# Performance work log

Measured on AMD Instinct MI355X. Metric: run time of the kernel, lower is better.

## Reference

```python
import jax, jax.numpy as jnp
import numpy as np

B, N, C = 128, 100, 32
HE = 32          # n_hidden_edge
FILTERS = [64, 64, 64]
OUT = 16


def setup_inputs() -> dict:
    key = jax.random.key(0)
    ks = jax.random.split(key, 16)
    x = jax.random.normal(ks[0], (B, N, C), dtype=jnp.float32)
    A = jax.random.uniform(ks[1], (B, N, N), dtype=jnp.float32)
    A = 0.5 * (A + A.transpose(0, 2, 1))  # symmetric adjacency
    mask = jnp.ones((B, N), dtype=jnp.float32)

    def lin(k, fin, fout):
        return jax.random.normal(k, (fin, fout), dtype=jnp.float32) / np.sqrt(fin).astype(np.float32)

    # edge_pred: Linear(2C -> HE), ReLU, Linear(HE -> 1)
    ew1 = lin(ks[2], 2 * C, HE); eb1 = jnp.zeros((HE,), jnp.float32)
    ew2 = lin(ks[3], HE, 1)[:, 0]; eb2 = jnp.zeros((), jnp.float32)
    # gconv layers: in = prev*2 relations (input A + predicted A)
    gw0 = lin(ks[4], C * 2, FILTERS[0]); gb0 = jnp.zeros((FILTERS[0],), jnp.float32)
    gw1 = lin(ks[5], FILTERS[0] * 2, FILTERS[1]); gb1 = jnp.zeros((FILTERS[1],), jnp.float32)
    gw2 = lin(ks[6], FILTERS[1] * 2, FILTERS[2]); gb2 = jnp.zeros((FILTERS[2],), jnp.float32)
    # final classifier (dropout is identity in eval mode)
    fw = lin(ks[7], FILTERS[2], OUT); fb = jnp.zeros((OUT,), jnp.float32)
    return dict(x=x, A=A, mask=mask, ew1=ew1, eb1=eb1, ew2=ew2, eb2=eb2,
                gw0=gw0, gb0=gb0, gw1=gw1, gb1=gb1, gw2=gw2, gb2=gb2, fw=fw, fb=fb)


def _laplacian(Ar):
    # K=1: A_hat = A + I; L = D^-1/2 A_hat D^-1/2 with D from sum over dim 1
    n = Ar.shape[1]
    A_hat = Ar + jnp.eye(n, dtype=Ar.dtype)[None]
    D = (jnp.sum(A_hat, axis=1) + 1e-5) ** (-0.5)  # [B,N]
    return D[:, :, None] * A_hat * D[:, None, :]


def reference(x, A, mask, ew1, eb1, ew2, eb2, gw0, gb0, gw1, gb1, gw2, gb2, fw, fb):
    Bv, Nv, Cv = x.shape
    # --- edge prediction over all valid pairs i<j (vectorized gather-MLP-scatter) ---
    # concat(x_i, x_j) @ ew1 factored: x_i @ ew1[:C] + x_j @ ew1[C:]
    hi = x @ ew1[:Cv]            # [B,N,HE]
    hj = x @ ew1[Cv:]            # [B,N,HE]
    pre = hi[:, :, None, :] + hj[:, None, :, :] + eb1      # [B,N,N,HE]
    h = jax.nn.relu(pre) @ ew2 + eb2                        # [B,N,N], h[b,i,j]=MLP([x_i,x_j])
    y = jnp.exp(0.5 * (h + h.transpose(0, 2, 1)))           # symmetric score
    valid = mask[:, :, None] * mask[:, None, :]
    triu = jnp.triu(jnp.ones((Nv, Nv), dtype=x.dtype), k=1)
    A_u = y * valid * triu                                  # scatter into upper triangle
    A_pred = A_u + A_u.transpose(0, 2, 1)

    # two relations: original A and predicted A
    L0 = _laplacian(A)
    L1 = _laplacian(A_pred)

    h = x
    for (W, b) in ((gw0, gb0), (gw1, gb1), (gw2, gb2)):
        xh = jnp.concatenate([L0 @ h, L1 @ h], axis=2)      # [B,N,2*F_in]
        h = jax.nn.relu((xh @ W + b) * mask[:, :, None])
    pooled = jnp.max(h, axis=1)                             # [B,F]
    return pooled @ fw + fb                                 # [B,OUT]
```

## Files before the change

### kernel.cpp

```cpp
#include <hip/hip_runtime.h>

#define NN 100
#define CC 32
#define HEE 32
#define FF 64
#define TILE 10

typedef float f32x4 __attribute__((ext_vector_type(4)));
typedef __bf16 bf16x8 __attribute__((ext_vector_type(8)));
#define MFMA16 __builtin_amdgcn_mfma_f32_16x16x32_bf16

union FragU {
  unsigned short s[8];
  bf16x8 v;
  float4 f4;
};

static __device__ __forceinline__ void split2(float v, unsigned short& h, unsigned short& l) {
  union { float f; unsigned u; } c; c.f = v;
  unsigned r = c.u + 0x7FFF + ((c.u >> 16) & 1);
  unsigned short hs = (unsigned short)(r >> 16);
  union { unsigned u; float f; } hb; hb.u = ((unsigned)hs) << 16;
  float rem = v - hb.f;
  union { float f; unsigned u; } c2; c2.f = rem;
  unsigned r2 = c2.u + 0x7FFF + ((c2.u >> 16) & 1);
  h = hs; l = (unsigned short)(r2 >> 16);
}

__global__ __launch_bounds__(64) void k_hidden(
    const float* __restrict__ x, const float* __restrict__ A,
    const float* __restrict__ ew1, const float* __restrict__ eb1,
    float* __restrict__ hi, float* __restrict__ hj, float* __restrict__ d0) {
  int bn = blockIdx.x;
  int t = threadIdx.x;
  __shared__ float xr[CC];
  if (t < CC) xr[t] = x[bn * CC + t];

  const float* arow = A + (size_t)bn * NN;
  float s = 0.f;
  for (int j = t; j < NN; j += 64) s += arow[j];
#pragma unroll
  for (int off = 32; off > 0; off >>= 1) s += __shfl_down(s, off);
  if (t == 0) d0[bn] = 1.0f / sqrtf(s + 1.0f + 1e-5f);

  __syncthreads();
  int k = t & 31;
  const float* w = ew1 + (t < 32 ? 0 : CC * HEE) + k;
  float acc = (t < 32) ? eb1[k] : 0.f;
#pragma unroll
  for (int c = 0; c < CC; ++c) acc += xr[c] * w[c * HEE];
  if (t < 32) hi[bn * HEE + k] = acc;
  else        hj[bn * HEE + k] = acc;
}

__global__ __launch_bounds__(256) void k_edge(
    const float* __restrict__ hi, const float* __restrict__ hj,
    const float* __restrict__ ew2, const float* __restrict__ eb2,
    const float* __restrict__ mask,
    float* __restrict__ Ahat1, float* __restrict__ d1) {
  __shared__ __align__(16) float shi[NN * HEE];
  __shared__ __align__(16) float shj[NN * HEE];
  __shared__ __align__(16) float sw2[HEE];
  __shared__ float sm[NN];
  __shared__ float sA[TILE][NN];
  int t = threadIdx.x;
  int b = blockIdx.x / 10;
  int i0 = (blockIdx.x % 10) * TILE;

  const float4* hi4 = (const float4*)(hi + (size_t)b * NN * HEE);
  const float4* hj4 = (const float4*)(hj + (size_t)b * NN * HEE);
  float4* shi4 = (float4*)shi;
  float4* shj4 = (float4*)shj;
  for (int v = t; v < NN * 8; v += 256) {
    int j = v >> 3, k4 = v & 7;
    int sw = (j << 3) | (k4 ^ (j & 7));
    shi4[sw] = hi4[v];
    shj4[sw] = hj4[v];
  }
  if (t < HEE) sw2[t] = ew2[t];
  if (t < NN) sm[t] = mask[b * NN + t];
  __syncthreads();

  float e2 = eb2[0];
  float4* sw24 = (float4*)sw2;
  for (int p = t; p < TILE * NN; p += 256) {
    int r = p / NN, j = p % NN, i = i0 + r;
    float val;
    if (j == i) {
      val = 1.0f;
    } else {
      float a1 = 0.f, a2 = 0.f;
#pragma unroll
      for (int k4 = 0; k4 < 8; ++k4) {
        float4 hii = shi4[(i << 3) | (k4 ^ (i & 7))];
        float4 hji = shj4[(i << 3) | (k4 ^ (i & 7))];
        float4 hij = shi4[(j << 3) | (k4 ^ (j & 7))];
        float4 hjj = shj4[(j << 3) | (k4 ^ (j & 7))];
        float4 w4 = sw24[k4];
        a1 += fmaxf(hii.x + hjj.x, 0.f) * w4.x;
        a2 += fmaxf(hij.x + hji.x, 0.f) * w4.x;
        a1 += fmaxf(hii.y + hjj.y, 0.f) * w4.y;
        a2 += fmaxf(hij.y + hji.y, 0.f) * w4.y;
        a1 += fmaxf(hii.z + hjj.z, 0.f) * w4.z;
        a2 += fmaxf(hij.z + hji.z, 0.f) * w4.z;
        a1 += fmaxf(hii.w + hjj.w, 0.f) * w4.w;
        a2 += fmaxf(hij.w + hji.w, 0.f) * w4.w;
      }
      val = expf(0.5f * (a1 + a2) + e2) * sm[i] * sm[j];
    }
    sA[r][j] = val;
    Ahat1[((size_t)b * NN + i) * NN + j] = val;
  }
  __syncthreads();
  if (t < TILE) {
    float s = 0.f;
    for (int j = 0; j < NN; ++j) s += sA[t][j];
    d1[b * NN + i0 + t] = 1.0f / sqrtf(s + 1e-5f);
  }
}

__global__ __launch_bounds__(256) void k_fmtL(
    const float* __restrict__ A, const float* __restrict__ Ahat1,
    const float* __restrict__ d0, const float* __restrict__ d1,
    float* __restrict__ Limg) {
  int gid = blockIdx.x * 256 + threadIdx.x;
  int lane = gid & 63;
  int frag = gid >> 6;
  int b = frag / 56;
  int r = frag % 56;
  int mt = r >> 3, kt = r & 7;
  int m = mt * 16 + (lane & 15);
  int o = lane >> 4;
  int rel = kt >> 2;
  int jb = (kt & 3) * 32 + o * 8;

  float v[8];
  if (m < NN) {
    if (rel == 0) {
      float di = d0[b * NN + m];
      const float* Ar = A + ((size_t)b * NN + m) * NN;
#pragma unroll
      for (int e = 0; e < 8; ++e) {
        int j = jb + e;
        v[e] = (j < NN) ? di * (Ar[j] + (j == m ? 1.f : 0.f)) * d0[b * NN + j] : 0.f;
      }
    } else {
      float di = d1[b * NN + m];
      const float* Ar = Ahat1 + ((size_t)b * NN + m) * NN;
#pragma unroll
      for (int e = 0; e < 8; ++e) {
        int j = jb + e;
        v[e] = (j < NN) ? di * Ar[j] * d1[b * NN + j] : 0.f;
      }
    }
  } else {
#pragma unroll
    for (int e = 0; e < 8; ++e) v[e] = 0.f;
  }
  FragU hh, ll;
#pragma unroll
  for (int e = 0; e < 8; ++e) split2(v[e], hh.s[e], ll.s[e]);
  char* dst = (char*)Limg + (size_t)frag * 2048 + lane * 16;
  *(float4*)dst = hh.f4;
  *(float4*)(dst + 1024) = ll.f4;
}

__global__ __launch_bounds__(256) void k_fmtW(
    const float* __restrict__ gw1, const float* __restrict__ gw2,
    float* __restrict__ Wimg) {
  int gid = blockIdx.x * 256 + threadIdx.x;
  int lane = gid & 63;
  int frag = gid >> 6;
  int wsel = frag >> 4;
  int rr = frag & 15;
  int kt2 = rr >> 3, nt2 = rr & 7;
  int n = nt2 * 16 + (lane & 15);
  int rel = n >> 6, f = n & 63;
  int kb = kt2 * 32 + (lane >> 4) * 8;
  const float* W = wsel ? gw2 : gw1;
  FragU hh, ll;
#pragma unroll
  for (int e = 0; e < 8; ++e) {
    float v = W[(size_t)(rel * 64 + kb + e) * 64 + f];
    split2(v, hh.s[e], ll.s[e]);
  }
  char* dst = (char*)Wimg + (size_t)frag * 2048 + lane * 16;
  *(float4*)dst = hh.f4;
  *(float4*)(dst + 1024) = ll.f4;
}

__global__ __launch_bounds__(256, 2) void k_preP(
    const float* __restrict__ x, const float* __restrict__ gw0,
    float* __restrict__ Pimg) {
  int t = threadIdx.x;
  int b = blockIdx.x & 127;
  int q = blockIdx.x >> 7;
  int wid = __builtin_amdgcn_readfirstlane(t >> 6);
  int lane = t & 63;
  int rg = wid * 4 + q;
  int row0 = rg * 8;
  if (row0 >= NN) return;

  int rowc[8];
#pragma unroll
  for (int r = 0; r < 8; ++r) rowc[r] = min(row0 + r, NN - 1);

  float acc0[8], acc1[8];
#pragma unroll
  for (int r = 0; r < 8; ++r) { acc0[r] = 0.f; acc1[r] = 0.f; }

  for (int c4 = 0; c4 < CC / 4; ++c4) {
    int c = c4 * 4;
    float w00 = gw0[(size_t)c * 64 + lane];
    float w01 = gw0[(size_t)(c + 1) * 64 + lane];
    float w02 = gw0[(size_t)(c + 2) * 64 + lane];
    float w03 = gw0[(size_t)(c + 3) * 64 + lane];
    float w10 = gw0[(size_t)(CC + c) * 64 + lane];
    float w11 = gw0[(size_t)(CC + c + 1) * 64 + lane];
    float w12 = gw0[(size_t)(CC + c + 2) * 64 + lane];
    float w13 = gw0[(size_t)(CC + c + 3) * 64 + lane];
#pragma unroll
    for (int r = 0; r < 8; ++r) {
      float4 a4 = *(const float4*)(x + ((size_t)b * NN + rowc[r]) * CC + c);
      acc0[r] += a4.x * w00 + a4.y * w01 + a4.z * w02 + a4.w * w03;
      acc1[r] += a4.x * w10 + a4.y * w11 + a4.z * w12 + a4.w * w13;
    }
  }
#pragma unroll
  for (int r = 0; r < 8; ++r) {
    if (row0 + r >= NN) { acc0[r] = 0.f; acc1[r] = 0.f; }
  }
  int o_t = (row0 & 31) >> 3;
  int lane_t = o_t * 16 + (lane & 15);
  int nt_t = lane >> 4;
  FragU h0, l0, h1, l1;
#pragma unroll
  for (int r = 0; r < 8; ++r) {
    split2(acc0[r], h0.s[r], l0.s[r]);
    split2(acc1[r], h1.s[r], l1.s[r]);
  }
  char* base = (char*)Pimg + (size_t)b * 65536;
  int kt0 = row0 >> 5;
  char* dp0 = base + (size_t)(kt0 * 4 + nt_t) * 2048 + lane_t * 16;
  *(float4*)dp0 = h0.f4;
  *(float4*)(dp0 + 1024) = l0.f4;
  char* dp1 = base + (size_t)((4 + kt0) * 4 + nt_t) * 2048 + lane_t * 16;
  *(float4*)dp1 = h1.f4;
  *(float4*)(dp1 + 1024) = l1.f4;
}

template <int LAST>
__global__ __launch_bounds__(256, 2) void k_gmm1(
    const float* __restrict__ Limg, const float* __restrict__ Pimg,
    const float* __restrict__ bias, const float* __restrict__ mask,
    float* __restrict__ outbuf, float* __restrict__ pooled) {
  __shared__ float pm[4][16];
  int t = threadIdx.x;
  int b = blockIdx.x >> 2;
  int q = blockIdx.x & 3;
  int h = q >> 1, np = q & 1;
  int w = __builtin_amdgcn_readfirstlane(t >> 6);
  int lane = t & 63;
  int nt = np * 2 + (w & 1);
  int mt0 = h * 3 + (w >> 1) * 2;
  int mt1 = mt0 + 1;

  const char* Lb = (const char*)Limg + (size_t)b * 114688;
  const char* Pb = (const char*)Pimg + (size_t)b * 65536;

  f32x4 acc0 = {0.f, 0.f, 0.f, 0.f};
  f32x4 acc1 = {0.f, 0.f, 0.f, 0.f};
#pragma unroll
  for (int kt = 0; kt < 8; ++kt) {
    FragU bh, bl, a0h, a0l, a1h, a1l;
    const char* pp = Pb + (size_t)(kt * 4 + nt) * 2048 + lane * 16;
    bh.f4 = *(const float4*)pp;
    bl.f4 = *(const float4*)(pp + 1024);
    const char* l0p = Lb + (size_t)(mt0 * 8 + kt) * 2048 + lane * 16;
    const char* l1p = Lb + (size_t)(mt1 * 8 + kt) * 2048 + lane * 16;
    a0h.f4 = *(const float4*)l0p;
    a0l.f4 = *(const float4*)(l0p + 1024);
    a1h.f4 = *(const float4*)l1p;
    a1l.f4 = *(const float4*)(l1p + 1024);
    acc0 = MFMA16(a0h.v, bh.v, acc0, 0, 0, 0);
    acc1 = MFMA16(a1h.v, bh.v, acc1, 0, 0, 0);
    acc0 = MFMA16(a0l.v, bh.v, acc0, 0, 0, 0);
    acc1 = MFMA16(a1l.v, bh.v, acc1, 0, 0, 0);
    acc0 = MFMA16(a0h.v, bl.v, acc0, 0, 0, 0);
    acc1 = MFMA16(a1h.v, bl.v, acc1, 0, 0, 0);
  }

  int f = nt * 16 + (lane & 15);
  float biasf = bias[f];
  const float* mb = mask + b * NN;
  int rbase = (lane >> 4) * 4;
  float mx = 0.f;

#pragma unroll
  for (int reg = 0; reg < 4; ++reg) {
    int gi = mt0 * 16 + rbase + reg;
    float v = 0.f;
    if (gi < NN) v = fmaxf((acc0[reg] + biasf) * mb[gi], 0.f);
    if (!LAST) outbuf[((size_t)b * 112 + gi) * 64 + f] = v;
    else mx = fmaxf(mx, v);
  }
#pragma unroll
  for (int reg = 0; reg < 4; ++reg) {
    int gi = mt1 * 16 + rbase + reg;
    float v = 0.f;
    if (gi < NN) v = fmaxf((acc1[reg] + biasf) * mb[gi], 0.f);
    if (!LAST) outbuf[((size_t)b * 112 + gi) * 64 + f] = v;
    else mx = fmaxf(mx, v);
  }

  if (LAST) {
    mx = fmaxf(mx, __shfl_xor(mx, 16));
    mx = fmaxf(mx, __shfl_xor(mx, 32));
    if (lane < 16) pm[w][lane] = mx;
    __syncthreads();
    if (w < 2 && lane < 16) {
      float m2 = fmaxf(pm[w][lane], pm[w + 2][lane]);
      pooled[((size_t)b * 2 + h) * 64 + (np * 2 + w) * 16 + lane] = m2;
    }
  }
}

__global__ __launch_bounds__(256, 2) void k_gmm2(
    const float* __restrict__ outbuf, const float* __restrict__ Wimg,
    float* __restrict__ Pimg_out) {
  int t = threadIdx.x;
  int b = blockIdx.x >> 2;
  int q2 = blockIdx.x & 3;
  int h = q2 >> 1, nh = q2 & 1;
  int w = __builtin_amdgcn_readfirstlane(t >> 6);
  int lane = t & 63;
  int nt2 = nh * 4 + w;
  int o = lane >> 4;
  int ml = lane & 15;

  f32x4 acc[4];
#pragma unroll
  for (int l = 0; l < 4; ++l) acc[l] = (f32x4){0.f, 0.f, 0.f, 0.f};

#pragma unroll
  for (int kt2 = 0; kt2 < 2; ++kt2) {
    FragU bh, bl;
    const char* wp = (const char*)Wimg + (size_t)(kt2 * 8 + nt2) * 2048 + lane * 16;
    bh.f4 = *(const float4*)wp;
    bl.f4 = *(const float4*)(wp + 1024);
    int kb = kt2 * 32 + o * 8;
#pragma unroll
    for (int l = 0; l < 4; ++l) {
      int m = (h * 3 + l) * 16 + ml;
      const float* op = outbuf + ((size_t)b * 112 + m) * 64 + kb;
      float4 v0 = *(const float4*)op;
      float4 v1 = *(const float4*)(op + 4);
      float vv[8] = {v0.x, v0.y, v0.z, v0.w, v1.x, v1.y, v1.z, v1.w};
      FragU ah, al;
#pragma unroll
      for (int e = 0; e < 8; ++e) split2(vv[e], ah.s[e], al.s[e]);
      acc[l] = MFMA16(ah.v, bh.v, acc[l], 0, 0, 0);
      acc[l] = MFMA16(al.v, bh.v, acc[l], 0, 0, 0);
      acc[l] = MFMA16(ah.v, bl.v, acc[l], 0, 0, 0);
    }
  }

  int nprime = nt2 * 16 + ml;
  int rel = nprime >> 6;
  int f = nprime & 63;
  int nt_t = f >> 4;
  char* Pout = (char*)Pimg_out + (size_t)b * 65536;
#pragma unroll
  for (int l = 0; l < 4; ++l) {
    int i0 = (h * 3 + l) * 16 + (lane >> 4) * 4;
    int kt_ = (rel * 128 + i0) >> 5;
    int o_t = ((rel * 128 + i0) & 31) >> 3;
    int e0 = i0 & 7;
    unsigned short hs[4], ls[4];
#pragma unroll
    for (int reg = 0; reg < 4; ++reg) split2(acc[l][reg], hs[reg], ls[reg]);
    ushort4 hv = {hs[0], hs[1], hs[2], hs[3]};
    ushort4 lv = {ls[0], ls[1], ls[2], ls[3]};
    char* dst = Pout + (size_t)(kt_ * 4 + nt_t) * 2048 + (o_t * 16 + (f & 15)) * 16 + e0 * 2;
    *(ushort4*)dst = hv;
    *(ushort4*)(dst + 1024) = lv;
  }
}

__global__ __launch_bounds__(64) void k_final(
    const float* __restrict__ pooled, const float* __restrict__ fw,
    const float* __restrict__ fb, float* __restrict__ out) {
  int b = blockIdx.x;
  int t = threadIdx.x;
  __shared__ float sp[FF];
  float m = fmaxf(pooled[(size_t)b * 128 + t], pooled[(size_t)b * 128 + 64 + t]);
  sp[t] = m;
  __syncthreads();
  if (t < 16) {
    float acc = fb[t];
#pragma unroll
    for (int f = 0; f < FF; ++f) acc += sp[f] * fw[f * 16 + t];
    out[b * 16 + t] = acc;
  }
}

extern "C" void kernel_launch(void* const* d_in, const int* in_sizes, int n_in,
                              void* d_out, int out_size, void* d_ws, size_t ws_size,
                              hipStream_t stream) {
  const float* x    = (const float*)d_in[0];
  const float* A    = (const float*)d_in[1];
  const float* mask = (const float*)d_in[2];
  const float* ew1  = (const float*)d_in[3];
  const float* eb1  = (const float*)d_in[4];
  const float* ew2  = (const float*)d_in[5];
  const float* eb2  = (const float*)d_in[6];
  const float* gw0  = (const float*)d_in[7];
  const float* gb0  = (const float*)d_in[8];
  const float* gw1  = (const float*)d_in[9];
  const float* gb1  = (const float*)d_in[10];
  const float* gw2  = (const float*)d_in[11];
  const float* gb2  = (const float*)d_in[12];
  const float* fw   = (const float*)d_in[13];
  const float* fb   = (const float*)d_in[14];
  float* out = (float*)d_out;
  float* ws = (float*)d_ws;

  const int B = 128;
  float* hi   = ws;
  float* hj   = hi + 409600;
  float* Ah1  = hj + 409600;
  float* d0   = Ah1 + 1280000;
  float* d1   = d0 + 12800;
  float* Limg = d1 + 12800;
  float* PA   = Limg + 3670016;
  float* PB   = PA + 2097152;
  float* Wimg = PB + 2097152;
  float* outb = Wimg + 16384;
  float* pooled = outb + 917504;

  k_hidden<<<B * NN, 64, 0, stream>>>(x, A, ew1, eb1, hi, hj, d0);
  k_edge<<<B * 10, 256, 0, stream>>>(hi, hj, ew2, eb2, mask, Ah1, d1);
  k_fmtW<<<8, 256, 0, stream>>>(gw1, gw2, Wimg);
  k_preP<<<512, 256, 0, stream>>>(x, gw0, PA);
  k_fmtL<<<1792, 256, 0, stream>>>(A, Ah1, d0, d1, Limg);

  k_gmm1<0><<<512, 256, 0, stream>>>(Limg, PA, gb0, mask, outb, pooled);
  k_gmm2<<<512, 256, 0, stream>>>(outb, (const float*)Wimg, PB);
  k_gmm1<0><<<512, 256, 0, stream>>>(Limg, PB, gb1, mask, outb, pooled);
  k_gmm2<<<512, 256, 0, stream>>>(outb, (const float*)((const char*)Wimg + 32768), PA);
  k_gmm1<1><<<512, 256, 0, stream>>>(Limg, PA, gb2, mask, outb, pooled);

  k_final<<<B, 64, 0, stream>>>(pooled, fw, fb, out);
}
```

Before: 92.61 us.

## Fuse prep kernels and merge per-layer graph GEMM with weight GEMM

Merges k_hidden, k_fmtW and k_preP into one k_combo launch, with k_hidden now handling four nodes per 256-thread block. k_edge is restructured so each 32-lane group owns one row, keeps the i-row hidden vectors in registers, and computes degree sums with shuffles instead of a serial loop. The two GEMM kernels per layer are fused into k_layer: the L·P result for a 16-row tile is staged in swizzled LDS and multiplied by the next weight image in place, removing the outbuf round trip and two launches. Pooling now writes seven partial maxima per batch, which k_final reduces. The trade-off is less MFMA work per block (one accumulator per wave) and some duplicated LDS staging.

Measured after the change: 101.3 us. 1.09x slower.

```diff
diff --git a/kernel.cpp b/kernel.cpp
--- a/kernel.cpp
+++ b/kernel.cpp
@@ -27,33 +27,122 @@
   h = hs; l = (unsigned short)(r2 >> 16);
 }
 
-__global__ __launch_bounds__(64) void k_hidden(
+__global__ __launch_bounds__(256) void k_combo(
     const float* __restrict__ x, const float* __restrict__ A,
     const float* __restrict__ ew1, const float* __restrict__ eb1,
-    float* __restrict__ hi, float* __restrict__ hj, float* __restrict__ d0) {
-  int bn = blockIdx.x;
+    const float* __restrict__ gw0, const float* __restrict__ gw1,
+    const float* __restrict__ gw2,
+    float* __restrict__ hi, float* __restrict__ hj, float* __restrict__ d0,
+    float* __restrict__ Wimg, float* __restrict__ Pimg) {
+  int blk = blockIdx.x;
   int t = threadIdx.x;
-  __shared__ float xr[CC];
-  if (t < CC) xr[t] = x[bn * CC + t];
-
-  const float* arow = A + (size_t)bn * NN;
-  float s = 0.f;
-  for (int j = t; j < NN; j += 64) s += arow[j];
-#pragma unroll
-  for (int off = 32; off > 0; off >>= 1) s += __shfl_down(s, off);
-  if (t == 0) d0[bn] = 1.0f / sqrtf(s + 1.0f + 1e-5f);
-
-  __syncthreads();
-  int k = t & 31;
-  const float* w = ew1 + (t < 32 ? 0 : CC * HEE) + k;
-  float acc = (t < 32) ? eb1[k] : 0.f;
-#pragma unroll
-  for (int c = 0; c < CC; ++c) acc += xr[c] * w[c * HEE];
-  if (t < 32) hi[bn * HEE + k] = acc;
-  else        hj[bn * HEE + k] = acc;
-}
-
-__global__ __launch_bounds__(256) void k_edge(
+
+  if (blk < 3200) {
+    __shared__ float xr[4][CC];
+    int wid = t >> 6, lane = t & 63;
+    int bn = blk * 4 + wid;
+    if (lane < CC) xr[wid][lane] = x[bn * CC + lane];
+
+    const float* arow = A + (size_t)bn * NN;
+    float s = arow[lane] + (lane < NN - 64 ? arow[lane + 64] : 0.f);
+#pragma unroll
+    for (int off = 32; off > 0; off >>= 1) s += __shfl_down(s, off);
+    if (lane == 0) d0[bn] = 1.0f / sqrtf(s + 1.0f + 1e-5f);
+    __syncthreads();
+
+    int k = lane & 31;
+    const float* w = ew1 + (lane < 32 ? 0 : CC * HEE) + k;
+    float acc = (lane < 32) ? eb1[k] : 0.f;
+#pragma unroll
+    for (int c = 0; c < CC; ++c) acc += xr[wid][c] * w[c * HEE];
+    if (lane < 32) hi[bn * HEE + k] = acc;
+    else           hj[bn * HEE + k] = acc;
+    return;
+  }
+
+  if (blk < 3208) {
+    int gid = (blk - 3200) * 256 + t;
+    int lane = gid & 63;
+    int frag = gid >> 6;
+    int wsel = frag >> 4;
+    int rr = frag & 15;
+    int kt2 = rr >> 3, nt2 = rr & 7;
+    int n = nt2 * 16 + (lane & 15);
+    int rel = n >> 6, f = n & 63;
+    int kb = kt2 * 32 + (lane >> 4) * 8;
+    const float* W = wsel ? gw2 : gw1;
+    FragU hh, ll;
+#pragma unroll
+    for (int e = 0; e < 8; ++e) {
+      float v = W[(size_t)(rel * 64 + kb + e) * 64 + f];
+      split2(v, hh.s[e], ll.s[e]);
+    }
+    char* dst = (char*)Wimg + (size_t)frag * 2048 + lane * 16;
+    *(float4*)dst = hh.f4;
+    *(float4*)(dst + 1024) = ll.f4;
+    return;
+  }
+
+  {
+    int idx = blk - 3208;
+    int b = idx & 127;
+    int q = idx >> 7;
+    int wid = t >> 6;
+    int lane = t & 63;
+    int rg = wid * 4 + q;
+    int row0 = rg * 8;
+    if (row0 >= NN) return;
+
+    int rowc[8];
+#pragma unroll
+    for (int r = 0; r < 8; ++r) rowc[r] = min(row0 + r, NN - 1);
+
+    float acc0[8], acc1[8];
+#pragma unroll
+    for (int r = 0; r < 8; ++r) { acc0[r] = 0.f; acc1[r] = 0.f; }
+
+    for (int c4 = 0; c4 < CC / 4; ++c4) {
+      int c = c4 * 4;
+      float w00 = gw0[(size_t)c * 64 + lane];
+      float w01 = gw0[(size_t)(c + 1) * 64 + lane];
+      float w02 = gw0[(size_t)(c + 2) * 64 + lane];
+      float w03 = gw0[(size_t)(c + 3) * 64 + lane];
+      float w10 = gw0[(size_t)(CC + c) * 64 + lane];
+      float w11 = gw0[(size_t)(CC + c + 1) * 64 + lane];
+      float w12 = gw0[(size_t)(CC + c + 2) * 64 + lane];
+      float w13 = gw0[(size_t)(CC + c + 3) * 64 + lane];
+#pragma unroll
+      for (int r = 0; r < 8; ++r) {
+        float4 a4 = *(const float4*)(x + ((size_t)b * NN + rowc[r]) * CC + c);
+        acc0[r] += a4.x * w00 + a4.y * w01 + a4.z * w02 + a4.w * w03;
+        acc1[r] += a4.x * w10 + a4.y * w11 + a4.z * w12 + a4.w * w13;
+      }
+    }
+#pragma unroll
+    for (int r = 0; r < 8; ++r) {
+      if (row0 + r >= NN) { acc0[r] = 0.f; acc1[r] = 0.f; }
+    }
+    int o_t = (row0 & 31) >> 3;
+    int lane_t = o_t * 16 + (lane & 15);
+    int nt_t = lane >> 4;
+    FragU h0, l0, h1, l1;
+#pragma unroll
+    for (int r = 0; r < 8; ++r) {
+      split2(acc0[r], h0.s[r], l0.s[r]);
+      split2(acc1[r], h1.s[r], l1.s[r]);
+    }
+    char* base = (char*)Pimg + (size_t)b * 65536;
+    int kt0 = row0 >> 5;
+    char* dp0 = base + (size_t)(kt0 * 4 + nt_t) * 2048 + lane_t * 16;
+    *(float4*)dp0 = h0.f4;
+    *(float4*)(dp0 + 1024) = l0.f4;
+    char* dp1 = base + (size_t)((4 + kt0) * 4 + nt_t) * 2048 + lane_t * 16;
+    *(float4*)dp1 = h1.f4;
+    *(float4*)(dp1 + 1024) = l1.f4;
+  }
+}
+
+__global__ __launch_bounds__(320) void k_edge(
     const float* __restrict__ hi, const float* __restrict__ hj,
     const float* __restrict__ ew2, const float* __restrict__ eb2,
     const float* __restrict__ mask,
@@ -62,7 +151,7 @@
   __shared__ __align__(16) float shj[NN * HEE];
   __shared__ __align__(16) float sw2[HEE];
   __shared__ float sm[NN];
-  __shared__ float sA[TILE][NN];
+  __shared__ float sA[TILE][NN + 4];
   int t = threadIdx.x;
   int b = blockIdx.x / 10;
   int i0 = (blockIdx.x % 10) * TILE;
@@ -71,7 +160,7 @@
   const float4* hj4 = (const float4*)(hj + (size_t)b * NN * HEE);
   float4* shi4 = (float4*)shi;
   float4* shj4 = (float4*)shj;
-  for (int v = t; v < NN * 8; v += 256) {
+  for (int v = t; v < NN * 8; v += 320) {
     int j = v >> 3, k4 = v & 7;
     int sw = (j << 3) | (k4 ^ (j & 7));
     shi4[sw] = hi4[v];
@@ -81,42 +170,55 @@
   if (t < NN) sm[t] = mask[b * NN + t];
   __syncthreads();
 
+  int r = t >> 5, jl = t & 31;
+  int i = i0 + r;
+  float4* sw24 = (float4*)sw2;
+
+  float4 hii[8], hji[8];
+#pragma unroll
+  for (int k4 = 0; k4 < 8; ++k4) {
+    int sw = (i << 3) | (k4 ^ (i & 7));
+    hii[k4] = shi4[sw];
+    hji[k4] = shj4[sw];
+  }
   float e2 = eb2[0];
-  float4* sw24 = (float4*)sw2;
-  for (int p = t; p < TILE * NN; p += 256) {
-    int r = p / NN, j = p % NN, i = i0 + r;
-    float val;
-    if (j == i) {
-      val = 1.0f;
-    } else {
+  float mi = sm[i];
+  float* Ar = Ahat1 + ((size_t)b * NN + i) * NN;
+
+#pragma unroll
+  for (int s = 0; s < 4; ++s) {
+    int j = jl + 32 * s;
+    if (j < NN) {
       float a1 = 0.f, a2 = 0.f;
 #pragma unroll
       for (int k4 = 0; k4 < 8; ++k4) {
-        float4 hii = shi4[(i << 3) | (k4 ^ (i & 7))];
-        float4 hji = shj4[(i << 3) | (k4 ^ (i & 7))];
-        float4 hij = shi4[(j << 3) | (k4 ^ (j & 7))];
-        float4 hjj = shj4[(j << 3) | (k4 ^ (j & 7))];
+        int sw = (j << 3) | (k4 ^ (j & 7));
+        float4 hjjK = shj4[sw];
+        float4 hijK = shi4[sw];
         float4 w4 = sw24[k4];
-        a1 += fmaxf(hii.x + hjj.x, 0.f) * w4.x;
-        a2 += fmaxf(hij.x + hji.x, 0.f) * w4.x;
-        a1 += fmaxf(hii.y + hjj.y, 0.f) * w4.y;
-        a2 += fmaxf(hij.y + hji.y, 0.f) * w4.y;
-        a1 += fmaxf(hii.z + hjj.z, 0.f) * w4.z;
-        a2 += fmaxf(hij.z + hji.z, 0.f) * w4.z;
-        a1 += fmaxf(hii.w + hjj.w, 0.f) * w4.w;
-        a2 += fmaxf(hij.w + hji.w, 0.f) * w4.w;
+        float4 hiiK = hii[k4], hjiK = hji[k4];
+        a1 += fmaxf(hiiK.x + hjjK.x, 0.f) * w4.x;
+        a2 += fmaxf(hijK.x + hjiK.x, 0.f) * w4.x;
+        a1 += fmaxf(hiiK.y + hjjK.y, 0.f) * w4.y;
+        a2 += fmaxf(hijK.y + hjiK.y, 0.f) * w4.y;
+        a1 += fmaxf(hiiK.z + hjjK.z, 0.f) * w4.z;
+        a2 += fmaxf(hijK.z + hjiK.z, 0.f) * w4.z;
+        a1 += fmaxf(hiiK.w + hjjK.w, 0.f) * w4.w;
+        a2 += fmaxf(hijK.w + hjiK.w, 0.f) * w4.w;
       }
-      val = expf(0.5f * (a1 + a2) + e2) * sm[i] * sm[j];
-    }
-    sA[r][j] = val;
-    Ahat1[((size_t)b * NN + i) * NN + j] = val;
+      float val = (j == i) ? 1.0f
+                           : expf(0.5f * (a1 + a2) + e2) * mi * sm[j];
+      sA[r][j] = val;
+      Ar[j] = val;
+    }
   }
   __syncthreads();
-  if (t < TILE) {
-    float s = 0.f;
-    for (int j = 0; j < NN; ++j) s += sA[t][j];
-    d1[b * NN + i0 + t] = 1.0f / sqrtf(s + 1e-5f);
-  }
+
+  float s2 = sA[r][jl] + sA[r][jl + 32] + sA[r][jl + 64] +
+             (jl < NN - 96 ? sA[r][jl + 96] : 0.f);
+#pragma unroll
+  for (int off = 16; off > 0; off >>= 1) s2 += __shfl_down(s2, off, 32);
+  if (jl == 0) d1[b * NN + i] = 1.0f / sqrtf(s2 + 1e-5f);
 }
 
 __global__ __launch_bounds__(256) void k_fmtL(
@@ -165,223 +267,112 @@
   *(float4*)(dst + 1024) = ll.f4;
 }
 
-__global__ __launch_bounds__(256) void k_fmtW(
-    const float* __restrict__ gw1, const float* __restrict__ gw2,
-    float* __restrict__ Wimg) {
-  int gid = blockIdx.x * 256 + threadIdx.x;
-  int lane = gid & 63;
-  int frag = gid >> 6;
-  int wsel = frag >> 4;
-  int rr = frag & 15;
-  int kt2 = rr >> 3, nt2 = rr & 7;
-  int n = nt2 * 16 + (lane & 15);
-  int rel = n >> 6, f = n & 63;
-  int kb = kt2 * 32 + (lane >> 4) * 8;
-  const float* W = wsel ? gw2 : gw1;
-  FragU hh, ll;
-#pragma unroll
-  for (int e = 0; e < 8; ++e) {
-    float v = W[(size_t)(rel * 64 + kb + e) * 64 + f];
-    split2(v, hh.s[e], ll.s[e]);
-  }
-  char* dst = (char*)Wimg + (size_t)frag * 2048 + lane * 16;
-  *(float4*)dst = hh.f4;
-  *(float4*)(dst + 1024) = ll.f4;
-}
-
-__global__ __launch_bounds__(256, 2) void k_preP(
-    const float* __restrict__ x, const float* __restrict__ gw0,
-    float* __restrict__ Pimg) {
-  int t = threadIdx.x;
-  int b = blockIdx.x & 127;
-  int q = blockIdx.x >> 7;
-  int wid = __builtin_amdgcn_readfirstlane(t >> 6);
-  int lane = t & 63;
-  int rg = wid * 4 + q;
-  int row0 = rg * 8;
-  if (row0 >= NN) return;
-
-  int rowc[8];
-#pragma unroll
-  for (int r = 0; r < 8; ++r) rowc[r] = min(row0 + r, NN - 1);
-
-  float acc0[8], acc1[8];
-#pragma unroll
-  for (int r = 0; r < 8; ++r) { acc0[r] = 0.f; acc1[r] = 0.f; }
-
-  for (int c4 = 0; c4 < CC / 4; ++c4) {
-    int c = c4 * 4;
-    float w00 = gw0[(size_t)c * 64 + lane];
-    float w01 = gw0[(size_t)(c + 1) * 64 + lane];
-    float w02 = gw0[(size_t)(c + 2) * 64 + lane];
-    float w03 = gw0[(size_t)(c + 3) * 64 + lane];
-    float w10 = gw0[(size_t)(CC + c) * 64 + lane];
-    float w11 = gw0[(size_t)(CC + c + 1) * 64 + lane];
-    float w12 = gw0[(size_t)(CC + c + 2) * 64 + lane];
-    float w13 = gw0[(size_t)(CC + c + 3) * 64 + lane];
-#pragma unroll
-    for (int r = 0; r < 8; ++r) {
-      float4 a4 = *(const float4*)(x + ((size_t)b * NN + rowc[r]) * CC + c);
-      acc0[r] += a4.x * w00 + a4.y * w01 + a4.z * w02 + a4.w * w03;
-      acc1[r] += a4.x * w10 + a4.y * w11 + a4.z * w12 + a4.w * w13;
-    }
-  }
-#pragma unroll
-  for (int r = 0; r < 8; ++r) {
-    if (row0 + r >= NN) { acc0[r] = 0.f; acc1[r] = 0.f; }
-  }
-  int o_t = (row0 & 31) >> 3;
-  int lane_t = o_t * 16 + (lane & 15);
-  int nt_t = lane >> 4;
-  FragU h0, l0, h1, l1;
-#pragma unroll
-  for (int r = 0; r < 8; ++r) {
-    split2(acc0[r], h0.s[r], l0.s[r]);
-    split2(acc1[r], h1.s[r], l1.s[r]);
-  }
-  char* base = (char*)Pimg + (size_t)b * 65536;
-  int kt0 = row0 >> 5;
-  char* dp0 = base + (size_t)(kt0 * 4 + nt_t) * 2048 + lane_t * 16;
-  *(float4*)dp0 = h0.f4;
-  *(float4*)(dp0 + 1024) = l0.f4;
-  char* dp1 = base + (size_t)((4 + kt0) * 4 + nt_t) * 2048 + lane_t * 16;
-  *(float4*)dp1 = h1.f4;
-  *(float4*)(dp1 + 1024) = l1.f4;
-}
-
 template <int LAST>
-__global__ __launch_bounds__(256, 2) void k_gmm1(
+__global__ __launch_bounds__(256) void k_layer(
     const float* __restrict__ Limg, const float* __restrict__ Pimg,
     const float* __restrict__ bias, const float* __restrict__ mask,
-    float* __restrict__ outbuf, float* __restrict__ pooled) {
-  __shared__ float pm[4][16];
+    const char* __restrict__ Wimg, float* __restrict__ Pout,
+    float* __restrict__ pooled) {
+  __shared__ __align__(16) float sO[16 * 64];
   int t = threadIdx.x;
-  int b = blockIdx.x >> 2;
-  int q = blockIdx.x & 3;
-  int h = q >> 1, np = q & 1;
-  int w = __builtin_amdgcn_readfirstlane(t >> 6);
+  int b = blockIdx.x / 7;
+  int mt = blockIdx.x % 7;
+  int w = t >> 6;
   int lane = t & 63;
-  int nt = np * 2 + (w & 1);
-  int mt0 = h * 3 + (w >> 1) * 2;
-  int mt1 = mt0 + 1;
+  int nt = w;
 
   const char* Lb = (const char*)Limg + (size_t)b * 114688;
   const char* Pb = (const char*)Pimg + (size_t)b * 65536;
 
-  f32x4 acc0 = {0.f, 0.f, 0.f, 0.f};
-  f32x4 acc1 = {0.f, 0.f, 0.f, 0.f};
+  f32x4 acc = {0.f, 0.f, 0.f, 0.f};
 #pragma unroll
   for (int kt = 0; kt < 8; ++kt) {
-    FragU bh, bl, a0h, a0l, a1h, a1l;
+    FragU bh, bl, ah, al;
     const char* pp = Pb + (size_t)(kt * 4 + nt) * 2048 + lane * 16;
     bh.f4 = *(const float4*)pp;
     bl.f4 = *(const float4*)(pp + 1024);
-    const char* l0p = Lb + (size_t)(mt0 * 8 + kt) * 2048 + lane * 16;
-    const char* l1p = Lb + (size_t)(mt1 * 8 + kt) * 2048 + lane * 16;
-    a0h.f4 = *(const float4*)l0p;
-    a0l.f4 = *(const float4*)(l0p + 1024);
-    a1h.f4 = *(const float4*)l1p;
-    a1l.f4 = *(const float4*)(l1p + 1024);
-    acc0 = MFMA16(a0h.v, bh.v, acc0, 0, 0, 0);
-    acc1 = MFMA16(a1h.v, bh.v, acc1, 0, 0, 0);
-    acc0 = MFMA16(a0l.v, bh.v, acc0, 0, 0, 0);
-    acc1 = MFMA16(a1l.v, bh.v, acc1, 0, 0, 0);
-    acc0 = MFMA16(a0h.v, bl.v, acc0, 0, 0, 0);
-    acc1 = MFMA16(a1h.v, bl.v, acc1, 0, 0, 0);
+    const char* lp = Lb + (size_t)(mt * 8 + kt) * 2048 + lane * 16;
+    ah.f4 = *(const float4*)lp;
+    al.f4 = *(const float4*)(lp + 1024);
+    acc = MFMA16(ah.v, bh.v, acc, 0, 0, 0);
+    acc = MFMA16(al.v, bh.v, acc, 0, 0, 0);
+    acc = MFMA16(ah.v, bl.v, acc, 0, 0, 0);
   }
 
   int f = nt * 16 + (lane & 15);
   float biasf = bias[f];
   const float* mb = mask + b * NN;
   int rbase = (lane >> 4) * 4;
-  float mx = 0.f;
-
+  float vv[4];
 #pragma unroll
   for (int reg = 0; reg < 4; ++reg) {
-    int gi = mt0 * 16 + rbase + reg;
-    float v = 0.f;
-    if (gi < NN) v = fmaxf((acc0[reg] + biasf) * mb[gi], 0.f);
-    if (!LAST) outbuf[((size_t)b * 112 + gi) * 64 + f] = v;
-    else mx = fmaxf(mx, v);
-  }
-#pragma unroll
-  for (int reg = 0; reg < 4; ++reg) {
-    int gi = mt1 * 16 + rbase + reg;
-    float v = 0.f;
-    if (gi < NN) v = fmaxf((acc1[reg] + biasf) * mb[gi], 0.f);
-    if (!LAST) outbuf[((size_t)b * 112 + gi) * 64 + f] = v;
-    else mx = fmaxf(mx, v);
+    int gi = mt * 16 + rbase + reg;
+    vv[reg] = (gi < NN) ? fmaxf((acc[reg] + biasf) * mb[gi], 0.f) : 0.f;
   }
 
   if (LAST) {
+    float mx = fmaxf(fmaxf(vv[0], vv[1]), fmaxf(vv[2], vv[3]));
     mx = fmaxf(mx, __shfl_xor(mx, 16));
     mx = fmaxf(mx, __shfl_xor(mx, 32));
-    if (lane < 16) pm[w][lane] = mx;
-    __syncthreads();
-    if (w < 2 && lane < 16) {
-      float m2 = fmaxf(pm[w][lane], pm[w + 2][lane]);
-      pooled[((size_t)b * 2 + h) * 64 + (np * 2 + w) * 16 + lane] = m2;
-    }
-  }
-}
-
-__global__ __launch_bounds__(256, 2) void k_gmm2(
-    const float* __restrict__ outbuf, const float* __restrict__ Wimg,
-    float* __restrict__ Pimg_out) {
-  int t = threadIdx.x;
-  int b = blockIdx.x >> 2;
-  int q2 = blockIdx.x & 3;
-  int h = q2 >> 1, nh = q2 & 1;
-  int w = __builtin_amdgcn_readfirstlane(t >> 6);
-  int lane = t & 63;
-  int nt2 = nh * 4 + w;
-  int o = lane >> 4;
-  int ml = lane & 15;
-
-  f32x4 acc[4];
-#pragma unroll
-  for (int l = 0; l < 4; ++l) acc[l] = (f32x4){0.f, 0.f, 0.f, 0.f};
-
+    if (lane < 16) pooled[((size_t)b * 7 + mt) * 64 + w * 16 + lane] = mx;
+    return;
+  }
+
+#pragma unroll
+  for (int reg = 0; reg < 4; ++reg) {
+    int lr2 = rbase + reg;
+    sO[lr2 * 64 + ((((f >> 3) ^ (lr2 & 7)) << 3) | (f & 7))] = vv[reg];
+  }
+  __syncthreads();
+
+  int ml = lane & 15, o = lane >> 4;
+  f32x4 accE0 = {0.f, 0.f, 0.f, 0.f};
+  f32x4 accE1 = {0.f, 0.f, 0.f, 0.f};
 #pragma unroll
   for (int kt2 = 0; kt2 < 2; ++kt2) {
-    FragU bh, bl;
-    const char* wp = (const char*)Wimg + (size_t)(kt2 * 8 + nt2) * 2048 + lane * 16;
-    bh.f4 = *(const float4*)wp;
-    bl.f4 = *(const float4*)(wp + 1024);
-    int kb = kt2 * 32 + o * 8;
-#pragma unroll
-    for (int l = 0; l < 4; ++l) {
-      int m = (h * 3 + l) * 16 + ml;
-      const float* op = outbuf + ((size_t)b * 112 + m) * 64 + kb;
-      float4 v0 = *(const float4*)op;
-      float4 v1 = *(const float4*)(op + 4);
-      float vv[8] = {v0.x, v0.y, v0.z, v0.w, v1.x, v1.y, v1.z, v1.w};
-      FragU ah, al;
-#pragma unroll
-      for (int e = 0; e < 8; ++e) split2(vv[e], ah.s[e], al.s[e]);
-      acc[l] = MFMA16(ah.v, bh.v, acc[l], 0, 0, 0);
-      acc[l] = MFMA16(al.v, bh.v, acc[l], 0, 0, 0);
-      acc[l] = MFMA16(ah.v, bl.v, acc[l], 0, 0, 0);
-    }
-  }
-
-  int nprime = nt2 * 16 + ml;
-  int rel = nprime >> 6;
-  int f = nprime & 63;
-  int nt_t = f >> 4;
-  char* Pout = (char*)Pimg_out + (size_t)b * 65536;
-#pragma unroll
-  for (int l = 0; l < 4; ++l) {
-    int i0 = (h * 3 + l) * 16 + (lane >> 4) * 4;
-    int kt_ = (rel * 128 + i0) >> 5;
-    int o_t = ((rel * 128 + i0) & 31) >> 3;
-    int e0 = i0 & 7;
+    int c = kt2 * 4 + o;
+    int cp = c ^ (ml & 7);
+    const float* op = &sO[ml * 64 + (cp << 3)];
+    float4 v0 = *(const float4*)op;
+    float4 v1 = *(const float4*)(op + 4);
+    float ve[8] = {v0.x, v0.y, v0.z, v0.w, v1.x, v1.y, v1.z, v1.w};
+    FragU ah, al;
+#pragma unroll
+    for (int e = 0; e < 8; ++e) split2(ve[e], ah.s[e], al.s[e]);
+    const char* wp0 = Wimg + (size_t)(kt2 * 8 + 2 * w) * 2048 + lane * 16;
+    const char* wp1 = Wimg + (size_t)(kt2 * 8 + 2 * w + 1) * 2048 + lane * 16;
+    FragU b0h, b0l, b1h, b1l;
+    b0h.f4 = *(const float4*)wp0;
+    b0l.f4 = *(const float4*)(wp0 + 1024);
+    b1h.f4 = *(const float4*)wp1;
+    b1l.f4 = *(const float4*)(wp1 + 1024);
+    accE0 = MFMA16(ah.v, b0h.v, accE0, 0, 0, 0);
+    accE0 = MFMA16(al.v, b0h.v, accE0, 0, 0, 0);
+    accE0 = MFMA16(ah.v, b0l.v, accE0, 0, 0, 0);
+    accE1 = MFMA16(ah.v, b1h.v, accE1, 0, 0, 0);
+    accE1 = MFMA16(al.v, b1h.v, accE1, 0, 0, 0);
+    accE1 = MFMA16(ah.v, b1l.v, accE1, 0, 0, 0);
+  }
+
+  char* Pob = (char*)Pout + (size_t)b * 65536;
+  int i0r = mt * 16 + o * 4;
+#pragma unroll
+  for (int half = 0; half < 2; ++half) {
+    f32x4 aE = half ? accE1 : accE0;
+    int nt2 = 2 * w + half;
+    int np = nt2 * 16 + ml;
+    int rel = np >> 6;
+    int fp = np & 63;
+    int kk = rel * 128 + i0r;
+    int kt_ = kk >> 5;
+    int o_t = (kk & 31) >> 3;
+    int e0 = i0r & 7;
     unsigned short hs[4], ls[4];
 #pragma unroll
-    for (int reg = 0; reg < 4; ++reg) split2(acc[l][reg], hs[reg], ls[reg]);
+    for (int reg = 0; reg < 4; ++reg) split2(aE[reg], hs[reg], ls[reg]);
     ushort4 hv = {hs[0], hs[1], hs[2], hs[3]};
     ushort4 lv = {ls[0], ls[1], ls[2], ls[3]};
-    char* dst = Pout + (size_t)(kt_ * 4 + nt_t) * 2048 + (o_t * 16 + (f & 15)) * 16 + e0 * 2;
+    char* dst = Pob + (size_t)(kt_ * 4 + (fp >> 4)) * 2048 + (o_t * 16 + (fp & 15)) * 16 + e0 * 2;
     *(ushort4*)dst = hv;
     *(ushort4*)(dst + 1024) = lv;
   }
@@ -393,7 +384,10 @@
   int b = blockIdx.x;
   int t = threadIdx.x;
   __shared__ float sp[FF];
-  float m = fmaxf(pooled[(size_t)b * 128 + t], pooled[(size_t)b * 128 + 64 + t]);
+  float m = -3.402823466e38f;
+  const float* pb = pooled + (size_t)b * 7 * 64;
+#pragma unroll
+  for (int rg = 0; rg < 7; ++rg) m = fmaxf(m, pb[rg * 64 + t]);
   sp[t] = m;
   __syncthreads();
   if (t < 16) {
@@ -435,20 +429,16 @@
   float* PA   = Limg + 3670016;
   float* PB   = PA + 2097152;
   float* Wimg = PB + 2097152;
-  float* outb = Wimg + 16384;
-  float* pooled = outb + 917504;
-
-  k_hidden<<<B * NN, 64, 0, stream>>>(x, A, ew1, eb1, hi, hj, d0);
-  k_edge<<<B * 10, 256, 0, stream>>>(hi, hj, ew2, eb2, mask, Ah1, d1);
-  k_fmtW<<<8, 256, 0, stream>>>(gw1, gw2, Wimg);
-  k_preP<<<512, 256, 0, stream>>>(x, gw0, PA);
+  float* pooled = Wimg + 16384;
+
+  k_combo<<<3720, 256, 0, stream>>>(x, A, ew1, eb1, gw0, gw1, gw2,
+                                    hi, hj, d0, Wimg, PA);
+  k_edge<<<B * 10, 320, 0, stream>>>(hi, hj, ew2, eb2, mask, Ah1, d1);
   k_fmtL<<<1792, 256, 0, stream>>>(A, Ah1, d0, d1, Limg);
 
-  k_gmm1<0><<<512, 256, 0, stream>>>(Limg, PA, gb0, mask, outb, pooled);
-  k_gmm2<<<512, 256, 0, stream>>>(outb, (const float*)Wimg, PB);
-  k_gmm1<0><<<512, 256, 0, stream>>>(Limg, PB, gb1, mask, outb, pooled);
-  k_gmm2<<<512, 256, 0, stream>>>(outb, (const float*)((const char*)Wimg + 32768), PA);
-  k_gmm1<1><<<512, 256, 0, stream>>>(Limg, PA, gb2, mask, outb, pooled);
+  k_layer<0><<<B * 7, 256, 0, stream>>>(Limg, PA, gb0, mask, (const char*)Wimg, PB, pooled);
+  k_layer<0><<<B * 7, 256, 0, stream>>>(Limg, PB, gb1, mask, (const char*)Wimg + 32768, PA, pooled);
+  k_layer<1><<<B * 7, 256, 0, stream>>>(Limg, PA, gb2, mask, (const char*)Wimg, PB, pooled);
 
   k_final<<<B, 64, 0, stream>>>(pooled, fw, fb, out);
 }
```
